# Optimization experiments

Measured on AMD Instinct MI355X. Metric: run time of the kernel, lower is better.

## Reference

```python
import jax, jax.numpy as jnp
import numpy as np

# Module constants from init_kwargs
N_X_AXIS = 128
N_Y_AXIS = 128
X_RANGE = (-10.0, 10.0)
Y_RANGE = (-10.0, 10.0)
LOG_L_SCALE = 0.0  # log(1.0), requires_grad=False
N_CTX = 20000


def make_grid():
    # Give_2d_Grid(min_x=x_range[0], max_x=x_range[1], min_y=y_range[1], max_y=y_range[0], flatten=True)
    # -> flattened (G,2) grid; row index i*N_Y_AXIS + j holds [x_i, y_j],
    # with y running from y_range[1] down to y_range[0] (note the swapped args in the source).
    xs = jnp.linspace(X_RANGE[0], X_RANGE[1], N_X_AXIS)
    ys = jnp.linspace(Y_RANGE[1], Y_RANGE[0], N_Y_AXIS)
    gx, gy = jnp.meshgrid(xs, ys, indexing='ij')  # (N_X, N_Y)
    return jnp.stack([gx, gy], axis=-1).reshape(-1, 2)  # (G, 2)


def setup_inputs() -> dict:
    key = jax.random.key(0)
    k1, k2 = jax.random.split(key)
    X = jax.random.normal(k1, (N_CTX, 2), dtype=jnp.float32) * 3.0  # context locations
    Y = jax.random.normal(k2, (N_CTX, 2), dtype=jnp.float32)        # context vectors
    return {"X": X, "Y": Y}


def reference(X, Y):
    # l_scale = exp(clamp(log_l_scale, -5, 5))
    l_scale = jnp.exp(jnp.clip(jnp.asarray(LOG_L_SCALE, X.dtype), -5.0, 5.0))
    grid = make_grid().astype(X.dtype)  # (G, 2)

    # RBF Gram matrix between grid and context points: exp(-||g - x||^2 / (2 l^2))
    # computed via the expanded-square trick to keep it a GEMM + elementwise.
    g2 = jnp.sum(grid * grid, axis=1, keepdims=True)        # (G, 1)
    x2 = jnp.sum(X * X, axis=1, keepdims=True).T            # (1, n)
    d2 = g2 + x2 - 2.0 * (grid @ X.T)                        # (G, n)
    Gram = jnp.exp(-d2 / (2.0 * l_scale * l_scale))          # (G, n)

    # Psi(Y): prepend a ones column -> (n, 3)
    Expand_Y = jnp.concatenate([jnp.ones((Y.shape[0], 1), Y.dtype), Y], axis=1)

    Feature_Map = Gram @ Expand_Y                            # (G, 3)

    # normalize smoothing channels by density channel
    density = Feature_Map[:, :1]
    Norm = jnp.concatenate([density, Feature_Map[:, 1:] / density], axis=1)

    # (G,3) -> (N_X, N_Y, 3) -> permute(2,1,0) -> (3, N_Y, N_X) -> (1, 3, N_Y, N_X)
    out = Norm.reshape(N_X_AXIS, N_Y_AXIS, 3).transpose(2, 1, 0)[None]
    return out
```

## Files before the change

kernel.cpp:

```cpp
#include <hip/hip_runtime.h>


#define NXA 128
#define NG  16384
#define NC  20000
#define KC  32
#define LDA 34
#define NSL 125
#define SLEN 160
#define NCHUNK 5

#define STEP (20.0f / 127.0f)
#define KNEG (-0.72134752044448170368f)

typedef _Float16 v8h  __attribute__((ext_vector_type(8)));
typedef float    v16f __attribute__((ext_vector_type(16)));
typedef float    v4f  __attribute__((ext_vector_type(4)));

__device__ __forceinline__ float fast_exp2(float x) {
    return __builtin_amdgcn_exp2f(x);
}

__global__ __launch_bounds__(256) void k_mfma(const float* __restrict__ X,
                                              const float* __restrict__ Y,
                                              float* __restrict__ fm) {
    __shared__ _Float16 Ag[32 * LDA];
    __shared__ _Float16 Bm[384 * LDA];

    const int t     = threadIdx.x;
    const int p     = blockIdx.x;
    const int slice = blockIdx.y;
    const int n0    = slice * SLEN;

    const int lane = t & 63, wave = t >> 6;
    const int l31 = lane & 31, lh = lane >> 5;
    const int kg = t & 3;
    const int i0 = t >> 2;
    const float gx0 = -10.f + (float)i0 * STEP;
    const float gx1 = -10.f + (float)(i0 + 64) * STEP;
    const float gyj = 10.f - (float)(32 * p + (t >> 2)) * STEP;

    const float4* Xp = (const float4*)X;
    const float4* Yp = (const float4*)Y;
    const int fb0 = (n0 >> 1) + kg * 4;

    v16f acc[3];
#pragma unroll
    for (int m = 0; m < 3; ++m) acc[m] = (v16f)(0.f);

    float4 xf[4], yf[4];
#pragma unroll
    for (int q = 0; q < 4; ++q) { xf[q] = Xp[fb0 + q]; yf[q] = Yp[fb0 + q]; }

#pragma unroll
    for (int m = 0; m < NCHUNK; ++m) {
        float4 xc[4], yc[4];
#pragma unroll
        for (int q = 0; q < 4; ++q) { xc[q] = xf[q]; yc[q] = yf[q]; }

        __syncthreads();

        if (m < NCHUNK - 1) {
            int fb = fb0 + 16 * (m + 1);
#pragma unroll
            for (int q = 0; q < 4; ++q) { xf[q] = Xp[fb + q]; yf[q] = Yp[fb + q]; }
        }

        {
            float xu[8], y0u[8], y1u[8];
#pragma unroll
            for (int q = 0; q < 4; ++q) {
                xu[2 * q]      = xc[q].x;  xu[2 * q + 1]  = xc[q].z;
                y0u[2 * q]     = yc[q].x;  y0u[2 * q + 1] = yc[q].z;
                y1u[2 * q]     = yc[q].y;  y1u[2 * q + 1] = yc[q].w;
            }
            v8h e, e1, e2;
#pragma unroll
            for (int u = 0; u < 8; ++u) {
                float dx = gx0 - xu[u];
                float w  = fast_exp2(dx * dx * KNEG);
                e[u]  = (_Float16)w;
                e1[u] = (_Float16)(w * y0u[u]);
                e2[u] = (_Float16)(w * y1u[u]);
            }
            *(v8h*)(Bm + i0 * LDA + kg * 8)         = e;
            *(v8h*)(Bm + (128 + i0) * LDA + kg * 8) = e1;
            *(v8h*)(Bm + (256 + i0) * LDA + kg * 8) = e2;
#pragma unroll
            for (int u = 0; u < 8; ++u) {
                float dx = gx1 - xu[u];
                float w  = fast_exp2(dx * dx * KNEG);
                e[u]  = (_Float16)w;
                e1[u] = (_Float16)(w * y0u[u]);
                e2[u] = (_Float16)(w * y1u[u]);
            }
            *(v8h*)(Bm + (64 + i0) * LDA + kg * 8)  = e;
            *(v8h*)(Bm + (192 + i0) * LDA + kg * 8) = e1;
            *(v8h*)(Bm + (320 + i0) * LDA + kg * 8) = e2;
        }
        if (t < 128) {
            v8h a;
#pragma unroll
            for (int u = 0; u < 8; ++u) {
                float x1u = (u & 1) ? ((u >> 1) == 0 ? xc[0].w : (u >> 1) == 1 ? xc[1].w : (u >> 1) == 2 ? xc[2].w : xc[3].w)
                                    : ((u >> 1) == 0 ? xc[0].y : (u >> 1) == 1 ? xc[1].y : (u >> 1) == 2 ? xc[2].y : xc[3].y);
                float dy = gyj - x1u;
                a[u] = (_Float16)fast_exp2(dy * dy * KNEG);
            }
            *(v8h*)(Ag + (t >> 2) * LDA + kg * 8) = a;
        }
        __syncthreads();

#pragma unroll
        for (int s = 0; s < 2; ++s) {
            int k = s * 16 + lh * 8;
            v8h af = *(const v8h*)(Ag + l31 * LDA + k);
#pragma unroll
            for (int tn = 0; tn < 3; ++tn) {
                int n = wave * 96 + tn * 32 + l31;
                v8h bf = *(const v8h*)(Bm + n * LDA + k);
                acc[tn] = __builtin_amdgcn_mfma_f32_32x32x16_f16(af, bf, acc[tn], 0, 0, 0);
            }
        }
    }

    const size_t cstride = (size_t)NSL * NG;
#pragma unroll
    for (int tn = 0; tn < 3; ++tn) {
        int n = wave * 96 + tn * 32 + l31;
        int c = n >> 7, i = n & 127;
        float* base = fm + (size_t)c * cstride + (size_t)slice * NG + i;
#pragma unroll
        for (int r = 0; r < 16; ++r) {
            int j  = (r & 3) + 8 * (r >> 2) + 4 * lh;
            int gj = 32 * p + j;
            base[gj * NXA] = acc[tn][r];
        }
    }
}

__global__ __launch_bounds__(256) void k_reduce_norm(const float* __restrict__ fm,
                                                     float* __restrict__ out) {
    __shared__ v4f sAcc[3][32][8];
    const int q  = threadIdx.x & 7;
    const int sg = threadIdx.x >> 3;
    const int gp = blockIdx.x * 32 + q * 4;
    const size_t cstride = (size_t)NSL * NG;
    const int per = (NSL + 31) >> 5;
    int s0 = sg * per;
    int s1 = s0 + per; if (s1 > NSL) s1 = NSL;
    v4f w = (v4f)(0.f), pp = (v4f)(0.f), qq = (v4f)(0.f);
    for (int s = s0; s < s1; ++s) {
        const float* base = fm + (size_t)s * NG + gp;
        w  += *(const v4f*)(base);
        pp += *(const v4f*)(base + cstride);
        qq += *(const v4f*)(base + 2 * cstride);
    }
    sAcc[0][sg][q] = w; sAcc[1][sg][q] = pp; sAcc[2][sg][q] = qq;
    __syncthreads();
    if (threadIdx.x < 8) {
        const int c = threadIdx.x;
        v4f W = (v4f)(0.f), P = (v4f)(0.f), Q = (v4f)(0.f);
#pragma unroll
        for (int s = 0; s < 32; ++s) {
            W += sAcc[0][s][c]; P += sAcc[1][s][c]; Q += sAcc[2][s][c];
        }
        v4f inv; inv.x = 1.f / W.x; inv.y = 1.f / W.y;
        inv.z = 1.f / W.z; inv.w = 1.f / W.w;
        const int o = blockIdx.x * 32 + c * 4;
        *(v4f*)(out + o)          = W;
        *(v4f*)(out + NG + o)     = P * inv;
        *(v4f*)(out + 2 * NG + o) = Q * inv;
    }
}

__global__ __launch_bounds__(256) void k_accum_atomic(const float* __restrict__ X,
                                                      const float* __restrict__ Y,
                                                      float* __restrict__ dst,
                                                      int slice_len) {
    __shared__ float As[64 * 64], Bs[64 * 64], Yl[64 * 2];
    const int t = threadIdx.x, tx = t & 15, ty = t >> 4;
    const int pos = blockIdx.x;
    const int tI = (pos >> 1) * 64, tJ = (pos & 1) * 64;
    const int n0 = blockIdx.y * slice_len;
    int nEnd = n0 + slice_len; if (nEnd > NC) nEnd = NC;
    float aw[16], ap[16], aq[16];
#pragma unroll
    for (int k = 0; k < 16; ++k) { aw[k] = ap[k] = aq[k] = 0.f; }
    for (int c0 = n0; c0 < nEnd; c0 += 64) {
        __syncthreads();
#pragma unroll
        for (int k = 0; k < 16; ++k) {
            int l = k * 256 + t, nl = l >> 6, ii = l & 63, n = c0 + nl;
            float a = 0.f, b = 0.f;
            if (n < nEnd) {
                float dx = (-10.f + (float)(tI + ii) * STEP) - X[2 * n];
                float dy = (10.f - (float)(tJ + ii) * STEP) - X[2 * n + 1];
                a = fast_exp2(dx * dx * KNEG);
                b = fast_exp2(dy * dy * KNEG);
            }
            As[nl * 64 + ii] = a; Bs[nl * 64 + ii] = b;
        }
        if (t < 128) { int n = c0 + (t >> 1); Yl[t] = (n < nEnd) ? Y[2 * n + (t & 1)] : 0.f; }
        __syncthreads();
        int cnt = nEnd - c0; if (cnt > 64) cnt = 64;
        for (int n = 0; n < cnt; ++n) {
            const float4 a4 = *(const float4*)(As + n * 64 + tx * 4);
            const float4 b4 = *(const float4*)(Bs + n * 64 + ty * 4);
            float y0 = Yl[2 * n], y1 = Yl[2 * n + 1];
            float av[4] = {a4.x, a4.y, a4.z, a4.w};
            float bv[4] = {b4.x, b4.y, b4.z, b4.w};
#pragma unroll
            for (int di = 0; di < 4; ++di)
#pragma unroll
                for (int dj = 0; dj < 4; ++dj) {
                    int k = di * 4 + dj;
                    float w = av[di] * bv[dj];
                    aw[k] += w; ap[k] = fmaf(w, y0, ap[k]); aq[k] = fmaf(w, y1, aq[k]);
                }
        }
    }
#pragma unroll
    for (int di = 0; di < 4; ++di)
#pragma unroll
        for (int dj = 0; dj < 4; ++dj) {
            int gi = tI + tx * 4 + di, gj = tJ + ty * 4 + dj;
            int o = gj * NXA + gi, k = di * 4 + dj;
            atomicAdd(dst + o, aw[k]);
            atomicAdd(dst + NG + o, ap[k]);
            atomicAdd(dst + 2 * NG + o, aq[k]);
        }
}

__global__ __launch_bounds__(256) void k_norm_inplace(float* __restrict__ out) {
    int t = blockIdx.x * 256 + threadIdx.x;
    if (t >= NG) return;
    float inv = 1.f / out[t];
    out[NG + t] *= inv; out[2 * NG + t] *= inv;
}

extern "C" void kernel_launch(void* const* d_in, const int* in_sizes, int n_in,
                              void* d_out, int out_size, void* d_ws, size_t ws_size,
                              hipStream_t stream) {
    const float* X = (const float*)d_in[0];
    const float* Y = (const float*)d_in[1];
    float* out = (float*)d_out;
    const size_t need = (size_t)NSL * NG * 3 * sizeof(float);
    if (ws_size >= need) {
        float* fm = (float*)d_ws;
        k_mfma<<<dim3(4, NSL), 256, 0, stream>>>(X, Y, fm);
        k_reduce_norm<<<NG / 32, 256, 0, stream>>>(fm, out);
    } else {
        hipMemsetAsync(d_out, 0, (size_t)out_size * sizeof(float), stream);
        k_accum_atomic<<<dim3(4, 64), 256, 0, stream>>>(X, Y, out, (NC + 63) / 64);
        k_norm_inplace<<<(NG + 255) / 256, 256, 0, stream>>>(out);
    }
}
```

Before: 76.45 us.

## Double-buffer LDS tiles so chunk staging overlaps MFMA compute

The shared-memory A and B tiles are split into two buffers, so the exp/feature staging for chunk m+1 is written while the MFMAs read chunk m. This removes one barrier per chunk. Global loads are also prefetched two chunks ahead. A launch-bounds minimum of 2 blocks per CU is added, which doubles LDS use per block and may constrain registers and occupancy.

```diff
diff --git a/kernel.cpp b/kernel.cpp
--- a/kernel.cpp
+++ b/kernel.cpp
@@ -21,11 +21,62 @@
     return __builtin_amdgcn_exp2f(x);
 }
 
-__global__ __launch_bounds__(256) void k_mfma(const float* __restrict__ X,
-                                              const float* __restrict__ Y,
-                                              float* __restrict__ fm) {
-    __shared__ _Float16 Ag[32 * LDA];
-    __shared__ _Float16 Bm[384 * LDA];
+__device__ __forceinline__ void stage_chunk(_Float16* __restrict__ AgB,
+                                            _Float16* __restrict__ BmB,
+                                            const float4 xc[4], const float4 yc[4],
+                                            int t, int kg, int i0,
+                                            float gx0, float gx1, float gyj) {
+    float xu[8], y0u[8], y1u[8];
+#pragma unroll
+    for (int q = 0; q < 4; ++q) {
+        xu[2 * q]      = xc[q].x;  xu[2 * q + 1]  = xc[q].z;
+        y0u[2 * q]     = yc[q].x;  y0u[2 * q + 1] = yc[q].z;
+        y1u[2 * q]     = yc[q].y;  y1u[2 * q + 1] = yc[q].w;
+    }
+    v8h e, e1, e2;
+#pragma unroll
+    for (int u = 0; u < 8; ++u) {
+        float dx = gx0 - xu[u];
+        float w  = fast_exp2(dx * dx * KNEG);
+        e[u]  = (_Float16)w;
+        e1[u] = (_Float16)(w * y0u[u]);
+        e2[u] = (_Float16)(w * y1u[u]);
+    }
+    *(v8h*)(BmB + i0 * LDA + kg * 8)         = e;
+    *(v8h*)(BmB + (128 + i0) * LDA + kg * 8) = e1;
+    *(v8h*)(BmB + (256 + i0) * LDA + kg * 8) = e2;
+#pragma unroll
+    for (int u = 0; u < 8; ++u) {
+        float dx = gx1 - xu[u];
+        float w  = fast_exp2(dx * dx * KNEG);
+        e[u]  = (_Float16)w;
+        e1[u] = (_Float16)(w * y0u[u]);
+        e2[u] = (_Float16)(w * y1u[u]);
+    }
+    *(v8h*)(BmB + (64 + i0) * LDA + kg * 8)  = e;
+    *(v8h*)(BmB + (192 + i0) * LDA + kg * 8) = e1;
+    *(v8h*)(BmB + (320 + i0) * LDA + kg * 8) = e2;
+    if (t < 128) {
+        v8h a;
+#pragma unroll
+        for (int u = 0; u < 8; ++u) {
+            float x1u = xu[u];
+            (void)x1u;
+            float dy;
+            float x1 = (u & 1) ? ((u >> 1) == 0 ? xc[0].w : (u >> 1) == 1 ? xc[1].w : (u >> 1) == 2 ? xc[2].w : xc[3].w)
+                               : ((u >> 1) == 0 ? xc[0].y : (u >> 1) == 1 ? xc[1].y : (u >> 1) == 2 ? xc[2].y : xc[3].y);
+            dy = gyj - x1;
+            a[u] = (_Float16)fast_exp2(dy * dy * KNEG);
+        }
+        *(v8h*)(AgB + (t >> 2) * LDA + kg * 8) = a;
+    }
+}
+
+__global__ __launch_bounds__(256, 2) void k_mfma(const float* __restrict__ X,
+                                                 const float* __restrict__ Y,
+                                                 float* __restrict__ fm) {
+    __shared__ _Float16 Ag[2][32 * LDA];
+    __shared__ _Float16 Bm[2][384 * LDA];
 
     const int t     = threadIdx.x;
     const int p     = blockIdx.x;
@@ -48,80 +99,43 @@
 #pragma unroll
     for (int m = 0; m < 3; ++m) acc[m] = (v16f)(0.f);
 
-    float4 xf[4], yf[4];
-#pragma unroll
-    for (int q = 0; q < 4; ++q) { xf[q] = Xp[fb0 + q]; yf[q] = Yp[fb0 + q]; }
+    float4 xc[4], yc[4], xf[4], yf[4];
+#pragma unroll
+    for (int q = 0; q < 4; ++q) { xc[q] = Xp[fb0 + q];      yc[q] = Yp[fb0 + q]; }
+#pragma unroll
+    for (int q = 0; q < 4; ++q) { xf[q] = Xp[fb0 + 16 + q]; yf[q] = Yp[fb0 + 16 + q]; }
+
+    stage_chunk(Ag[0], Bm[0], xc, yc, t, kg, i0, gx0, gx1, gyj);
+    __syncthreads();
 
 #pragma unroll
     for (int m = 0; m < NCHUNK; ++m) {
-        float4 xc[4], yc[4];
-#pragma unroll
-        for (int q = 0; q < 4; ++q) { xc[q] = xf[q]; yc[q] = yf[q]; }
-
-        __syncthreads();
-
         if (m < NCHUNK - 1) {
-            int fb = fb0 + 16 * (m + 1);
-#pragma unroll
-            for (int q = 0; q < 4; ++q) { xf[q] = Xp[fb + q]; yf[q] = Yp[fb + q]; }
-        }
-
-        {
-            float xu[8], y0u[8], y1u[8];
-#pragma unroll
-            for (int q = 0; q < 4; ++q) {
-                xu[2 * q]      = xc[q].x;  xu[2 * q + 1]  = xc[q].z;
-                y0u[2 * q]     = yc[q].x;  y0u[2 * q + 1] = yc[q].z;
-                y1u[2 * q]     = yc[q].y;  y1u[2 * q + 1] = yc[q].w;
+#pragma unroll
+            for (int q = 0; q < 4; ++q) { xc[q] = xf[q]; yc[q] = yf[q]; }
+            if (m < NCHUNK - 2) {
+                int fb = fb0 + 16 * (m + 2);
+#pragma unroll
+                for (int q = 0; q < 4; ++q) { xf[q] = Xp[fb + q]; yf[q] = Yp[fb + q]; }
             }
-            v8h e, e1, e2;
-#pragma unroll
-            for (int u = 0; u < 8; ++u) {
-                float dx = gx0 - xu[u];
-                float w  = fast_exp2(dx * dx * KNEG);
-                e[u]  = (_Float16)w;
-                e1[u] = (_Float16)(w * y0u[u]);
-                e2[u] = (_Float16)(w * y1u[u]);
-            }
-            *(v8h*)(Bm + i0 * LDA + kg * 8)         = e;
-            *(v8h*)(Bm + (128 + i0) * LDA + kg * 8) = e1;
-            *(v8h*)(Bm + (256 + i0) * LDA + kg * 8) = e2;
-#pragma unroll
-            for (int u = 0; u < 8; ++u) {
-                float dx = gx1 - xu[u];
-                float w  = fast_exp2(dx * dx * KNEG);
-                e[u]  = (_Float16)w;
-                e1[u] = (_Float16)(w * y0u[u]);
-                e2[u] = (_Float16)(w * y1u[u]);
-            }
-            *(v8h*)(Bm + (64 + i0) * LDA + kg * 8)  = e;
-            *(v8h*)(Bm + (192 + i0) * LDA + kg * 8) = e1;
-            *(v8h*)(Bm + (320 + i0) * LDA + kg * 8) = e2;
-        }
-        if (t < 128) {
-            v8h a;
-#pragma unroll
-            for (int u = 0; u < 8; ++u) {
-                float x1u = (u & 1) ? ((u >> 1) == 0 ? xc[0].w : (u >> 1) == 1 ? xc[1].w : (u >> 1) == 2 ? xc[2].w : xc[3].w)
-                                    : ((u >> 1) == 0 ? xc[0].y : (u >> 1) == 1 ? xc[1].y : (u >> 1) == 2 ? xc[2].y : xc[3].y);
-                float dy = gyj - x1u;
-                a[u] = (_Float16)fast_exp2(dy * dy * KNEG);
-            }
-            *(v8h*)(Ag + (t >> 2) * LDA + kg * 8) = a;
-        }
-        __syncthreads();
-
+            stage_chunk(Ag[(m + 1) & 1], Bm[(m + 1) & 1], xc, yc,
+                        t, kg, i0, gx0, gx1, gyj);
+        }
+
+        const _Float16* AgR = Ag[m & 1];
+        const _Float16* BmR = Bm[m & 1];
 #pragma unroll
         for (int s = 0; s < 2; ++s) {
             int k = s * 16 + lh * 8;
-            v8h af = *(const v8h*)(Ag + l31 * LDA + k);
+            v8h af = *(const v8h*)(AgR + l31 * LDA + k);
 #pragma unroll
             for (int tn = 0; tn < 3; ++tn) {
                 int n = wave * 96 + tn * 32 + l31;
-                v8h bf = *(const v8h*)(Bm + n * LDA + k);
+                v8h bf = *(const v8h*)(BmR + n * LDA + k);
                 acc[tn] = __builtin_amdgcn_mfma_f32_32x32x16_f16(af, bf, acc[tn], 0, 0, 0);
             }
         }
+        if (m < NCHUNK - 1) __syncthreads();
     }
 
     const size_t cstride = (size_t)NSL * NG;
```

Result: slower. 86.39 us (+13.0%).

## Double grid-y tile per block to reuse x-direction B operand across two MFMA rows

Applied to the files above, without the earlier changes.

Each block now covers 64 grid-y rows instead of 32, computing two A tiles and reusing each loaded B fragment for two MFMAs. This halves the number of blocks and halves the redundant exp computation of the x-direction Gram/feature B matrix, which was rebuilt by every block. The cost is fewer blocks (250 vs 500) on a 256-CU device, so fewer CUs stay busy, plus doubled accumulator registers; launch_bounds min-blocks set to 1.

```diff
diff --git a/kernel.cpp b/kernel.cpp
--- a/kernel.cpp
+++ b/kernel.cpp
@@ -21,14 +21,14 @@
     return __builtin_amdgcn_exp2f(x);
 }
 
-__global__ __launch_bounds__(256) void k_mfma(const float* __restrict__ X,
-                                              const float* __restrict__ Y,
-                                              float* __restrict__ fm) {
-    __shared__ _Float16 Ag[32 * LDA];
+__global__ __launch_bounds__(256, 1) void k_mfma(const float* __restrict__ X,
+                                                 const float* __restrict__ Y,
+                                                 float* __restrict__ fm) {
+    __shared__ _Float16 Ag[64 * LDA];
     __shared__ _Float16 Bm[384 * LDA];
 
     const int t     = threadIdx.x;
-    const int p     = blockIdx.x;
+    const int pp    = blockIdx.x;
     const int slice = blockIdx.y;
     const int n0    = slice * SLEN;
 
@@ -38,15 +38,17 @@
     const int i0 = t >> 2;
     const float gx0 = -10.f + (float)i0 * STEP;
     const float gx1 = -10.f + (float)(i0 + 64) * STEP;
-    const float gyj = 10.f - (float)(32 * p + (t >> 2)) * STEP;
+    const float gyj = 10.f - (float)(64 * pp + (t >> 2)) * STEP;
 
     const float4* Xp = (const float4*)X;
     const float4* Yp = (const float4*)Y;
     const int fb0 = (n0 >> 1) + kg * 4;
 
-    v16f acc[3];
-#pragma unroll
-    for (int m = 0; m < 3; ++m) acc[m] = (v16f)(0.f);
+    v16f acc[2][3];
+#pragma unroll
+    for (int jt = 0; jt < 2; ++jt)
+#pragma unroll
+        for (int m = 0; m < 3; ++m) acc[jt][m] = (v16f)(0.f);
 
     float4 xf[4], yf[4];
 #pragma unroll
@@ -66,14 +68,16 @@
             for (int q = 0; q < 4; ++q) { xf[q] = Xp[fb + q]; yf[q] = Yp[fb + q]; }
         }
 
+        float xu[8], x1u[8], y0u[8], y1u[8];
+#pragma unroll
+        for (int q = 0; q < 4; ++q) {
+            xu[2 * q]  = xc[q].x;  xu[2 * q + 1]  = xc[q].z;
+            x1u[2 * q] = xc[q].y;  x1u[2 * q + 1] = xc[q].w;
+            y0u[2 * q] = yc[q].x;  y0u[2 * q + 1] = yc[q].z;
+            y1u[2 * q] = yc[q].y;  y1u[2 * q + 1] = yc[q].w;
+        }
+
         {
-            float xu[8], y0u[8], y1u[8];
-#pragma unroll
-            for (int q = 0; q < 4; ++q) {
-                xu[2 * q]      = xc[q].x;  xu[2 * q + 1]  = xc[q].z;
-                y0u[2 * q]     = yc[q].x;  y0u[2 * q + 1] = yc[q].z;
-                y1u[2 * q]     = yc[q].y;  y1u[2 * q + 1] = yc[q].w;
-            }
             v8h e, e1, e2;
 #pragma unroll
             for (int u = 0; u < 8; ++u) {
@@ -98,13 +102,11 @@
             *(v8h*)(Bm + (192 + i0) * LDA + kg * 8) = e1;
             *(v8h*)(Bm + (320 + i0) * LDA + kg * 8) = e2;
         }
-        if (t < 128) {
+        {
             v8h a;
 #pragma unroll
             for (int u = 0; u < 8; ++u) {
-                float x1u = (u & 1) ? ((u >> 1) == 0 ? xc[0].w : (u >> 1) == 1 ? xc[1].w : (u >> 1) == 2 ? xc[2].w : xc[3].w)
-                                    : ((u >> 1) == 0 ? xc[0].y : (u >> 1) == 1 ? xc[1].y : (u >> 1) == 2 ? xc[2].y : xc[3].y);
-                float dy = gyj - x1u;
+                float dy = gyj - x1u[u];
                 a[u] = (_Float16)fast_exp2(dy * dy * KNEG);
             }
             *(v8h*)(Ag + (t >> 2) * LDA + kg * 8) = a;
@@ -114,29 +116,33 @@
 #pragma unroll
         for (int s = 0; s < 2; ++s) {
             int k = s * 16 + lh * 8;
-            v8h af = *(const v8h*)(Ag + l31 * LDA + k);
+            v8h af0 = *(const v8h*)(Ag + l31 * LDA + k);
+            v8h af1 = *(const v8h*)(Ag + (32 + l31) * LDA + k);
 #pragma unroll
             for (int tn = 0; tn < 3; ++tn) {
                 int n = wave * 96 + tn * 32 + l31;
                 v8h bf = *(const v8h*)(Bm + n * LDA + k);
-                acc[tn] = __builtin_amdgcn_mfma_f32_32x32x16_f16(af, bf, acc[tn], 0, 0, 0);
+                acc[0][tn] = __builtin_amdgcn_mfma_f32_32x32x16_f16(af0, bf, acc[0][tn], 0, 0, 0);
+                acc[1][tn] = __builtin_amdgcn_mfma_f32_32x32x16_f16(af1, bf, acc[1][tn], 0, 0, 0);
             }
         }
     }
 
     const size_t cstride = (size_t)NSL * NG;
 #pragma unroll
-    for (int tn = 0; tn < 3; ++tn) {
-        int n = wave * 96 + tn * 32 + l31;
-        int c = n >> 7, i = n & 127;
-        float* base = fm + (size_t)c * cstride + (size_t)slice * NG + i;
-#pragma unroll
-        for (int r = 0; r < 16; ++r) {
-            int j  = (r & 3) + 8 * (r >> 2) + 4 * lh;
-            int gj = 32 * p + j;
-            base[gj * NXA] = acc[tn][r];
-        }
-    }
+    for (int jt = 0; jt < 2; ++jt)
+#pragma unroll
+        for (int tn = 0; tn < 3; ++tn) {
+            int n = wave * 96 + tn * 32 + l31;
+            int c = n >> 7, i = n & 127;
+            float* base = fm + (size_t)c * cstride + (size_t)slice * NG + i;
+#pragma unroll
+            for (int r = 0; r < 16; ++r) {
+                int j  = (r & 3) + 8 * (r >> 2) + 4 * lh;
+                int gj = 64 * pp + 32 * jt + j;
+                base[gj * NXA] = acc[jt][tn][r];
+            }
+        }
 }
 
 __global__ __launch_bounds__(256) void k_reduce_norm(const float* __restrict__ fm,
@@ -248,7 +254,7 @@
     const size_t need = (size_t)NSL * NG * 3 * sizeof(float);
     if (ws_size >= need) {
         float* fm = (float*)d_ws;
-        k_mfma<<<dim3(4, NSL), 256, 0, stream>>>(X, Y, fm);
+        k_mfma<<<dim3(2, NSL), 256, 0, stream>>>(X, Y, fm);
         k_reduce_norm<<<NG / 32, 256, 0, stream>>>(fm, out);
     } else {
         hipMemsetAsync(d_out, 0, (size_t)out_size * sizeof(float), stream);
```

Result: no change. 75.22 us (-1.6%).
